# Performance work log

Hardware: AMD Instinct MI355X
Metric: run time of the kernel (lower is better)

The kernel has to match this reference:

```python
import jax, jax.numpy as jnp
import numpy as np
from jax import lax

B, C, H, W = 2, 64, 48, 64
RU, RV = 3, 3
U, V = 2 * RU + 1, 2 * RV + 1
D = U * V  # 49 displacements


def setup_inputs() -> dict:
    key = jax.random.key(0)
    ks = jax.random.split(key, 12)
    p = lambda k, shape, s: jax.random.normal(k, shape, jnp.float32) * s
    feat1 = p(ks[0], (B, C, H, W), 1.0)
    feat2 = p(ks[1], (B, C, H, W), 1.0)
    gy, gx = jnp.meshgrid(jnp.arange(H, dtype=jnp.float32), jnp.arange(W, dtype=jnp.float32), indexing='ij')
    base = jnp.broadcast_to(jnp.stack([gx, gy])[None], (B, 2, H, W))  # channel0=x, channel1=y
    coords = base + p(ks[2], (B, 2, H, W), 1.5)
    return {
        'feat1': feat1, 'feat2': feat2, 'coords': coords,
        # MatchingNet (ConvBlock = conv+ReLU, BN folded into conv)
        'w0': p(ks[3], (96, 2 * C, 3, 3), 0.06), 'b0': jnp.zeros((96,), jnp.float32),
        'w1': p(ks[4], (128, 96, 3, 3), 0.05), 'b1': jnp.zeros((128,), jnp.float32),
        'w2': p(ks[5], (128, 128, 3, 3), 0.04), 'b2': jnp.zeros((128,), jnp.float32),
        'w3': p(ks[6], (64, 128, 3, 3), 0.04), 'b3': jnp.zeros((64,), jnp.float32),
        'wd': p(ks[7], (32, 64, 4, 4), 0.05), 'bd': jnp.zeros((32,), jnp.float32),  # deconv k4 s2 p1
        'w5': p(ks[8], (1, 32, 3, 3), 0.1), 'b5': jnp.zeros((1,), jnp.float32),
        # Displacement-aware projection: 1x1 conv over the 49 displacement channels
        'wdap': p(ks[9], (D, D), 0.15),
    }


def _conv(x, w, b, stride=1, pad=1):
    y = lax.conv_general_dilated(x, w, (stride, stride), ((pad, pad), (pad, pad)),
                                 dimension_numbers=('NCHW', 'OIHW', 'NCHW'))
    return y + b[None, :, None, None]


def _warp_with_context(feat2, coords):
    # grid_sample(bilinear, zeros padding, align_corners=True) at coords + every displacement
    b, c, h, w = feat2.shape
    du = jnp.arange(-RU, RU + 1, dtype=feat2.dtype)
    dv = jnp.arange(-RV, RV + 1, dtype=feat2.dtype)
    x = coords[:, 0][:, None, None, :, :] + du[None, None, :, None, None]  # (b,V,U,h,w) via broadcast
    y = coords[:, 1][:, None, None, :, :] + dv[None, :, None, None, None]
    x0 = jnp.floor(x); y0 = jnp.floor(y)
    wx = (x - x0)[:, None]; wy = (y - y0)[:, None]  # (b,1,V,U,h,w)
    x0i = x0.astype(jnp.int32); y0i = y0.astype(jnp.int32)
    feat_flat = feat2.reshape(b, c, h * w)

    def gather(xi, yi):
        valid = (xi >= 0) & (xi < w) & (yi >= 0) & (yi < h)
        idx = jnp.clip(yi, 0, h - 1) * w + jnp.clip(xi, 0, w - 1)
        v = jax.vmap(lambda f, i: f[:, i])(feat_flat, idx.reshape(b, -1))  # (b,c,P)
        v = v.reshape(b, c, V, U, h, w)
        return v * valid[:, None].astype(feat2.dtype)

    v00 = gather(x0i, y0i)
    v01 = gather(x0i + 1, y0i)
    v10 = gather(x0i, y0i + 1)
    v11 = gather(x0i + 1, y0i + 1)
    out = v00 * (1 - wx) * (1 - wy) + v01 * wx * (1 - wy) + v10 * (1 - wx) * wy + v11 * wx * wy
    return out.transpose(0, 2, 3, 1, 4, 5)  # (b, V, U, c, h, w)


def reference(feat1, feat2, coords, w0, b0, w1, b1, w2, b2, w3, b3, wd, bd, w5, b5, wdap):
    b, c, h, w = feat1.shape
    f2 = _warp_with_context(feat2, coords)
    f1 = jnp.broadcast_to(feat1[:, None, None], (b, V, U, c, h, w))
    feat = jnp.concatenate([f1, f2], axis=3).reshape(b * V * U, 2 * c, h, w)
    # MatchingNet
    x = jnp.maximum(_conv(feat, w0, b0), 0)
    x = jnp.maximum(_conv(x, w1, b1, stride=2), 0)
    x = jnp.maximum(_conv(x, w2, b2), 0)
    x = jnp.maximum(_conv(x, w3, b3), 0)
    x = lax.conv_general_dilated(x, wd, (1, 1), ((2, 2), (2, 2)), lhs_dilation=(2, 2),
                                 dimension_numbers=('NCHW', 'OIHW', 'NCHW')) + bd[None, :, None, None]
    x = jnp.maximum(x, 0)
    cost = _conv(x, w5, b5).reshape(b, V, U, h, w)
    # DAP: 1x1 conv across the D displacement channels, no bias
    cost = jnp.einsum('ed,bdhw->behw', wdap, cost.reshape(b, D, h, w)).reshape(b, V, U, h, w)
    prob = jax.nn.softmax(cost.reshape(b, D, h, w), axis=1).reshape(b, V, U, h, w)
    du = jnp.arange(-RU, RU + 1, dtype=feat1.dtype)
    dv = jnp.arange(-RV, RV + 1, dtype=feat1.dtype)
    dx = jnp.sum(prob * du[None, None, :, None, None], axis=(1, 2))
    dy = jnp.sum(prob * dv[None, :, None, None, None], axis=(1, 2))
    return coords + jnp.stack([dx, dy], axis=1)
```

## Files before the change

kernel.cpp:

```cpp
#include <hip/hip_runtime.h>
#include <hip/hip_bf16.h>

using bf16 = __hip_bfloat16;
typedef __attribute__((ext_vector_type(8))) __bf16 bf16x8;
typedef __attribute__((ext_vector_type(4))) float f32x4;

static __device__ __forceinline__ bf16 f2b(float v) { return __float2bfloat16(v); }
static __device__ __forceinline__ float us2f(unsigned short u) {
    return __uint_as_float(((unsigned)u) << 16);
}


__global__ void sentinel_k(float* __restrict__ out, int nel, float val) {
    int i = blockIdx.x * 256 + threadIdx.x;
    if (i < nel) out[i] = val;
}

__global__ void pack_all(const float* __restrict__ w0, const float* __restrict__ w1,
                         const float* __restrict__ w2, const float* __restrict__ w3,
                         const float* __restrict__ wd, bf16* __restrict__ wsw0,
                         bf16* __restrict__ wsw0a, bf16* __restrict__ wsw1,
                         bf16* __restrict__ wsw2, bf16* __restrict__ wsw3,
                         bf16* __restrict__ wswd) {
    int i = blockIdx.x * 256 + threadIdx.x;
    if (i < 110592) {
        int icbase = (i < 55296) ? 64 : 0;
        bf16* dst = (i < 55296) ? wsw0 : wsw0a;
        int o = (i < 55296) ? i : i - 55296;
        int j = o & 7, lane = (o >> 3) & 63;
        int m = lane & 15, q = lane >> 4;
        int cc = (o >> 9) & 1;
        int fragid = o >> 10;
        int t = fragid / 6, ocf = fragid % 6;
        int oc = ocf * 16 + m, ic = cc * 32 + q * 8 + j;
        dst[o] = f2b(w0[((size_t)oc * 128 + icbase + ic) * 9 + t]);
    } else if (i < 307200) {
        int o = i - 110592;
        int j = o & 7, lane = (o >> 3) & 63;
        int m = lane & 15, q = lane >> 4;
        int cc = (o >> 9) % 12;
        int fragid = (o >> 9) / 12;
        int t2 = fragid / 8, ocf = fragid % 8;
        int oc = ocf * 16 + m;
        int pc = cc * 32 + q * 8 + j;
        int dy = (t2 < 2) ? -1 : 0;
        int dx = (t2 & 1) ? 0 : -1;
        int p = pc / 96, ic = pc % 96;
        int py = p >> 1, px = p & 1;
        int ky = (dy == -1) ? (py == 1 ? 0 : -1) : (py == 0 ? 1 : 2);
        int kx = (dx == -1) ? (px == 1 ? 0 : -1) : (px == 0 ? 1 : 2);
        float v = (ky >= 0 && kx >= 0) ? w1[((size_t)oc * 96 + ic) * 9 + ky * 3 + kx] : 0.f;
        wsw1[o] = f2b(v);
    } else if (i < 454656) {
        int o = i - 307200;
        int j = o & 7, lane = (o >> 3) & 63;
        int m = lane & 15, q = lane >> 4;
        int cc = (o >> 9) % 4;
        int fragid = (o >> 9) / 4;
        int t = fragid / 8, ocf = fragid % 8;
        int oc = ocf * 16 + m, ic = cc * 32 + q * 8 + j;
        wsw2[o] = f2b(w2[((size_t)oc * 128 + ic) * 9 + t]);
    } else if (i < 528384) {
        int o = i - 454656;
        int j = o & 7, lane = (o >> 3) & 63;
        int m = lane & 15, q = lane >> 4;
        int cc = (o >> 9) % 4;
        int fragid = (o >> 9) / 4;
        int t = fragid / 4, ocf = fragid % 4;
        int oc = ocf * 16 + m, ic = cc * 32 + q * 8 + j;
        wsw3[o] = f2b(w3[((size_t)oc * 128 + ic) * 9 + t]);
    } else if (i < 561152) {
        int o = i - 528384;
        int j = o & 7, lane = (o >> 3) & 63;
        int m = lane & 15, q = lane >> 4;
        int cc = (o >> 9) & 1;
        int ocf = (o >> 10) & 1;
        int t2 = (o >> 11) & 3;
        int c = o >> 13;
        int oc = ocf * 16 + m, ic = cc * 32 + q * 8 + j;
        int qy = c >> 1, qx = c & 1;
        int dy = qy - 1 + (t2 >> 1), dx = qx - 1 + (t2 & 1);
        int ky = (qy == 0) ? (dy == -1 ? 0 : 2) : (dy == 0 ? 1 : 3);
        int kx = (qx == 0) ? (dx == -1 ? 0 : 2) : (dx == 0 ? 1 : 3);
        wswd[o] = f2b(wd[((size_t)oc * 64 + ic) * 16 + ky * 4 + kx]);
    }
}

__global__ void to_nhwc2(const float* __restrict__ feat1, const float* __restrict__ feat2,
                         bf16* __restrict__ f1n, bf16* __restrict__ f2n) {
    int i = blockIdx.x * 256 + threadIdx.x;
    const float* src = (i < 393216) ? feat1 : feat2;
    bf16* dst = (i < 393216) ? f1n : f2n;
    int o = (i < 393216) ? i : i - 393216;
    if (o >= 393216) return;
    int c = o & 63;
    int p = (o >> 6) % 3072;
    int b = o / (3072 * 64);
    dst[o] = f2b(src[((size_t)b * 64 + c) * 3072 + p]);
}

__global__ __launch_bounds__(256) void warp_kernel(const bf16* __restrict__ f2n,
                                                   const float* __restrict__ coords,
                                                   bf16* __restrict__ f2w, int bd0, int cnt) {
    int idx = blockIdx.x * 256 + threadIdx.x;
    if (idx >= cnt * 3072 * 8) return;
    int g = idx & 7;
    int pix = idx >> 3;
    int p = pix % 3072;
    int z = pix / 3072;
    int bd = bd0 + z;
    int b = bd / 49, d = bd % 49;
    float du = (float)(d % 7 - 3), dv = (float)(d / 7 - 3);
    float cx = coords[(size_t)(b * 2 + 0) * 3072 + p] + du;
    float cy = coords[(size_t)(b * 2 + 1) * 3072 + p] + dv;
    float x0f = floorf(cx), y0f = floorf(cy);
    float wx = cx - x0f, wy = cy - y0f;
    int x0 = (int)x0f, y0 = (int)y0f;
    int x1 = x0 + 1, y1 = y0 + 1;
    bool vx0 = (x0 >= 0) && (x0 < 64), vx1 = (x1 >= 0) && (x1 < 64);
    bool vy0 = (y0 >= 0) && (y0 < 48), vy1 = (y1 >= 0) && (y1 < 48);
    int xc0 = min(max(x0, 0), 63), xc1 = min(max(x1, 0), 63);
    int yc0 = min(max(y0, 0), 47), yc1 = min(max(y1, 0), 47);
    float w00 = (vx0 && vy0) ? (1.f - wx) * (1.f - wy) : 0.f;
    float w01 = (vx1 && vy0) ? wx * (1.f - wy) : 0.f;
    float w10 = (vx0 && vy1) ? (1.f - wx) * wy : 0.f;
    float w11 = (vx1 && vy1) ? wx * wy : 0.f;
    const unsigned short* f2 = (const unsigned short*)f2n + (size_t)b * 3072 * 64 + g * 8;
    ushort4 a0 = *(const ushort4*)(f2 + (size_t)(yc0 * 64 + xc0) * 64);
    ushort4 a1 = *(const ushort4*)(f2 + (size_t)(yc0 * 64 + xc0) * 64 + 4);
    ushort4 b0v = *(const ushort4*)(f2 + (size_t)(yc0 * 64 + xc1) * 64);
    ushort4 b1v = *(const ushort4*)(f2 + (size_t)(yc0 * 64 + xc1) * 64 + 4);
    ushort4 c0 = *(const ushort4*)(f2 + (size_t)(yc1 * 64 + xc0) * 64);
    ushort4 c1 = *(const ushort4*)(f2 + (size_t)(yc1 * 64 + xc0) * 64 + 4);
    ushort4 d0 = *(const ushort4*)(f2 + (size_t)(yc1 * 64 + xc1) * 64);
    ushort4 d1 = *(const ushort4*)(f2 + (size_t)(yc1 * 64 + xc1) * 64 + 4);
    unsigned short ua[8] = {a0.x, a0.y, a0.z, a0.w, a1.x, a1.y, a1.z, a1.w};
    unsigned short ub[8] = {b0v.x, b0v.y, b0v.z, b0v.w, b1v.x, b1v.y, b1v.z, b1v.w};
    unsigned short uc[8] = {c0.x, c0.y, c0.z, c0.w, c1.x, c1.y, c1.z, c1.w};
    unsigned short ud[8] = {d0.x, d0.y, d0.z, d0.w, d1.x, d1.y, d1.z, d1.w};
    unsigned short ro[8];
#pragma unroll
    for (int e = 0; e < 8; ++e) {
        float v = w00 * us2f(ua[e]) + w01 * us2f(ub[e]) + w10 * us2f(uc[e]) + w11 * us2f(ud[e]);
        bf16 r = f2b(v);
        ro[e] = *(unsigned short*)&r;
    }
    unsigned short* outp = (unsigned short*)f2w + ((size_t)z * 3072 + p) * 64 + g * 8;
    *(ushort4*)outp = (ushort4){ro[0], ro[1], ro[2], ro[3]};
    *(ushort4*)(outp + 4) = (ushort4){ro[4], ro[5], ro[6], ro[7]};
}

template <int IC, int OCTOT, int OC_BLK, int H, int W, int MROWS, int NTAPS, int DXW,
          int DYLO, int DXLO, int BMODE, int OMODE>
__global__ __launch_bounds__(256, 4) void conv_px4(const bf16* __restrict__ in_,
                                                   const bf16* __restrict__ wsw_,
                                                   const float* __restrict__ bias,
                                                   const bf16* __restrict__ base_,
                                                   bf16* __restrict__ out, int bd0) {
    constexpr int NCH = IC / 32;
    constexpr int NfT = OC_BLK / 16;
    constexpr int TPXQ = MROWS * W / 4;
    constexpr int MF = TPXQ / 16;
    constexpr int NDY = NTAPS / DXW;
    constexpr int ROWS_IN = MROWS + NDY - 1;
    constexpr int COLS_IN = W + DXW - 1;
    constexpr int NOCF = OCTOT / 16;
    constexpr int PITCH = 40;
    constexpr int SZA = ROWS_IN * COLS_IN * PITCH;
    constexpr int OUTSH = MROWS * W * OC_BLK;
    constexpr int SMEM = (SZA > OUTSH) ? SZA : OUTSH;
    __shared__ __align__(16) unsigned short s_mem[SMEM];

    const unsigned short* in = (const unsigned short*)in_;
    const unsigned short* wsw = (const unsigned short*)wsw_;
    const unsigned short* baseh = (const unsigned short*)base_;
    const int tid = threadIdx.x;
    const int wp = tid >> 6, lane = tid & 63;
    const int m = lane & 15, q = lane >> 4;
    const int bx = blockIdx.x, by = blockIdx.y, z = blockIdx.z;
    const int foff = m * PITCH + q * 8;
    const int ocbase = by * OC_BLK;

    f32x4 acc[MF][NfT];
#pragma unroll
    for (int a = 0; a < MF; ++a)
#pragma unroll
        for (int nf = 0; nf < NfT; ++nf) acc[a][nf] = (f32x4){0.f, 0.f, 0.f, 0.f};

    for (int cc = 0; cc < NCH; ++cc) {
        constexpr int SZE = ROWS_IN * COLS_IN * 4;
        for (int i = tid; i < SZE; i += 256) {
            int e = i & 3;
            int pix = i >> 2;
            int cI = pix % COLS_IN;
            int rr = pix / COLS_IN;
            int gy = bx * MROWS + rr + DYLO;
            int gx = cI + DXLO;
            uint4 v = {0u, 0u, 0u, 0u};
            if (gy >= 0 && gy < H && gx >= 0 && gx < W)
                v = *(const uint4*)(in + ((size_t)(z * H + gy) * W + gx) * IC + cc * 32 + e * 8);
            *(uint4*)(&s_mem[pix * PITCH + e * 8]) = v;
        }
        __syncthreads();
        {
            bf16x8 bcur[NfT], bnxt[NfT];
#pragma unroll
            for (int nf = 0; nf < NfT; ++nf) {
                const int fragoc = (ocbase >> 4) + nf;
                bcur[nf] = *(const bf16x8*)(wsw + (((size_t)0 * NOCF + fragoc) * NCH + cc) * 512 +
                                            lane * 8);
            }
#pragma unroll
            for (int t = 0; t < NTAPS; ++t) {
                if (t + 1 < NTAPS) {
#pragma unroll
                    for (int nf = 0; nf < NfT; ++nf) {
                        const int fragoc = (ocbase >> 4) + nf;
                        bnxt[nf] = *(const bf16x8*)(wsw +
                                                    (((size_t)(t + 1) * NOCF + fragoc) * NCH + cc) *
                                                        512 +
                                                    lane * 8);
                    }
                }
                bf16x8 af[MF];
#pragma unroll
                for (int mf = 0; mf < MF; ++mf) {
                    const int pxb = wp * TPXQ + mf * 16;
                    const int yl = pxb / W, xb = pxb % W;
                    const unsigned short* pa =
                        &s_mem[((yl + t / DXW) * COLS_IN + xb + t % DXW) * PITCH] + foff;
                    af[mf] = *(const bf16x8*)pa;
                }
#pragma unroll
                for (int mf = 0; mf < MF; ++mf)
#pragma unroll
                    for (int nf = 0; nf < NfT; ++nf)
                        acc[mf][nf] = __builtin_amdgcn_mfma_f32_16x16x32_bf16(af[mf], bcur[nf],
                                                                              acc[mf][nf], 0, 0, 0);
                if (t + 1 < NTAPS) {
#pragma unroll
                    for (int nf = 0; nf < NfT; ++nf) bcur[nf] = bnxt[nf];
                }
            }
        }
        __syncthreads();
    }

    const int bimg = (bd0 + z) / 49;
    float bb[NfT];
    if constexpr (BMODE == 0) {
#pragma unroll
        for (int nf = 0; nf < NfT; ++nf) bb[nf] = bias[ocbase + nf * 16 + m];
    }
#pragma unroll
    for (int mf = 0; mf < MF; ++mf) {
        const int pxb = wp * TPXQ + mf * 16;
#pragma unroll
        for (int r = 0; r < 4; ++r) {
            const int px = pxb + q * 4 + r;
            const int yl = px / W, xl = px % W;
            const int gy = bx * MROWS + yl;
#pragma unroll
            for (int nf = 0; nf < NfT; ++nf) {
                const int oc = nf * 16 + m;
                float v = acc[mf][nf][r];
                if constexpr (BMODE == 1)
                    v += us2f(baseh[(((size_t)bimg * 48 + gy) * 64 + xl) * 96 + ocbase + oc]);
                else
                    v += bb[nf];
                if constexpr (OMODE != 4) v = fmaxf(v, 0.f);
                bf16 bv = f2b(v);
                s_mem[px * OC_BLK + oc] = *(unsigned short*)&bv;
            }
        }
    }
    __syncthreads();
    constexpr int TOT16 = MROWS * W * OC_BLK / 8;
    for (int g = tid; g < TOT16; g += 256) {
        const int o = g * 8;
        if constexpr (OMODE == 1) {
            const int xx = o / 384;
            const int rr = o % 384;
            const int pp = rr / 96;
            const int oco = rr % 96;
            const int px = (pp >> 1) * 64 + 2 * xx + (pp & 1);
            uint4 vv = *(const uint4*)&s_mem[px * 96 + oco];
            *(uint4*)((unsigned short*)out + (((size_t)z * 24 + bx) * 32 + xx) * 384 + rr) = vv;
        } else {
            uint4 vv = *(const uint4*)&s_mem[o];
            const int px = o / OC_BLK;
            const int oco = o % OC_BLK;
            const int gy = bx * MROWS + px / W;
            const int xl = px % W;
            *(uint4*)((unsigned short*)out + (((size_t)z * H + gy) * W + xl) * OCTOT + ocbase +
                      oco) = vv;
        }
    }
}

__global__ __launch_bounds__(256, 4) void deconv_c4(const bf16* __restrict__ in_,
                                                    const bf16* __restrict__ wswd_,
                                                    const float* __restrict__ bias,
                                                    bf16* __restrict__ out) {
    constexpr int PITCH = 40;
    __shared__ __align__(16) unsigned short s_mem[16384];

    const unsigned short* in = (const unsigned short*)in_;
    const unsigned short* wsw = (const unsigned short*)wswd_;
    const int tid = threadIdx.x;
    const int cls = tid >> 6, lane = tid & 63;
    const int m = lane & 15, q = lane >> 4;
    const int qy = cls >> 1, qx = cls & 1;
    const int bx = blockIdx.x;
    const int z = blockIdx.y;
    const int foff = m * PITCH + q * 8;

    f32x4 acc[8][2];
#pragma unroll
    for (int a = 0; a < 8; ++a) {
        acc[a][0] = (f32x4){0.f, 0.f, 0.f, 0.f};
        acc[a][1] = (f32x4){0.f, 0.f, 0.f, 0.f};
    }

    for (int cc = 0; cc < 2; ++cc) {
        constexpr int SZE = 6 * 34 * 4;
        for (int i = tid; i < SZE; i += 256) {
            int e = i & 3;
            int pix = i >> 2;
            int cI = pix % 34;
            int rr = pix / 34;
            int gy = bx * 4 + rr - 1;
            int gx = cI - 1;
            uint4 v = {0u, 0u, 0u, 0u};
            if (gy >= 0 && gy < 24 && gx >= 0 && gx < 32)
                v = *(const uint4*)(in + ((size_t)(z * 24 + gy) * 32 + gx) * 64 + cc * 32 + e * 8);
            *(uint4*)(&s_mem[pix * PITCH + e * 8]) = v;
        }
        __syncthreads();
        {
            bf16x8 bcur[2], bnxt[2];
#pragma unroll
            for (int nf = 0; nf < 2; ++nf)
                bcur[nf] = *(const bf16x8*)(wsw + cls * 8192 + nf * 1024 + cc * 512 + lane * 8);
#pragma unroll
            for (int t = 0; t < 4; ++t) {
                if (t + 1 < 4) {
#pragma unroll
                    for (int nf = 0; nf < 2; ++nf)
                        bnxt[nf] = *(const bf16x8*)(wsw + cls * 8192 + (t + 1) * 2048 + nf * 1024 +
                                                    cc * 512 + lane * 8);
                }
                const int dy = qy - 1 + (t >> 1);
                const int dx = qx - 1 + (t & 1);
                bf16x8 af[8];
#pragma unroll
                for (int mf = 0; mf < 8; ++mf) {
                    const int yl = mf >> 1, xb = (mf & 1) * 16;
                    const unsigned short* pa =
                        &s_mem[((yl + dy + 1) * 34 + xb + dx + 1) * PITCH] + foff;
                    af[mf] = *(const bf16x8*)pa;
                }
#pragma unroll
                for (int mf = 0; mf < 8; ++mf)
#pragma unroll
                    for (int nf = 0; nf < 2; ++nf)
                        acc[mf][nf] = __builtin_amdgcn_mfma_f32_16x16x32_bf16(af[mf], bcur[nf],
                                                                              acc[mf][nf], 0, 0, 0);
                if (t + 1 < 4) {
                    bcur[0] = bnxt[0];
                    bcur[1] = bnxt[1];
                }
            }
        }
        __syncthreads();
    }

    const float bb0 = bias[m], bb1 = bias[16 + m];
#pragma unroll
    for (int mf = 0; mf < 8; ++mf) {
#pragma unroll
        for (int r = 0; r < 4; ++r) {
            const int px = mf * 16 + q * 4 + r;
            const int yl = px >> 5, xl = px & 31;
            const int opx = (2 * yl + qy) * 64 + 2 * xl + qx;
            float v0 = fmaxf(acc[mf][0][r] + bb0, 0.f);
            float v1 = fmaxf(acc[mf][1][r] + bb1, 0.f);
            bf16 b0 = f2b(v0), b1 = f2b(v1);
            s_mem[opx * 32 + m] = *(unsigned short*)&b0;
            s_mem[opx * 32 + 16 + m] = *(unsigned short*)&b1;
        }
    }
    __syncthreads();
    for (int g = tid; g < 2048; g += 256) {
        const int o = g * 8;
        *(uint4*)((unsigned short*)out + ((size_t)z * 3072 + bx * 512) * 32 + o) =
            *(const uint4*)&s_mem[o];
    }
}

__global__ __launch_bounds__(256) void conv5_k(const bf16* __restrict__ in_,
                                               const float* __restrict__ w5,
                                               const float* __restrict__ b5,
                                               float* __restrict__ cost, int bd0, int cnt) {
    __shared__ float s_w5[9][32];
    const int tid = threadIdx.x;
    for (int i = tid; i < 288; i += 256) {
        int ic = i % 32, t = i / 32;
        s_w5[t][ic] = w5[ic * 9 + t];
    }
    __syncthreads();
    int idx = blockIdx.x * 256 + tid;
    if (idx >= cnt * 3072) return;
    int p = idx % 3072, z = idx / 3072;
    int y = p >> 6, x = p & 63;
    const unsigned short* in = (const unsigned short*)in_;
    float acc = b5[0];
#pragma unroll
    for (int ky = 0; ky < 3; ++ky) {
        int gy = y + ky - 1;
        if (gy < 0 || gy >= 48) continue;
#pragma unroll
        for (int kx = 0; kx < 3; ++kx) {
            int gx = x + kx - 1;
            if (gx < 0 || gx >= 64) continue;
            const ushort4* src = (const ushort4*)(in + ((size_t)(z * 48 + gy) * 64 + gx) * 32);
            const float* wr = s_w5[ky * 3 + kx];
#pragma unroll
            for (int e = 0; e < 8; ++e) {
                ushort4 u = src[e];
                acc = fmaf(us2f(u.x), wr[e * 4 + 0], acc);
                acc = fmaf(us2f(u.y), wr[e * 4 + 1], acc);
                acc = fmaf(us2f(u.z), wr[e * 4 + 2], acc);
                acc = fmaf(us2f(u.w), wr[e * 4 + 3], acc);
            }
        }
    }
    cost[(size_t)(bd0 + z) * 3072 + p] = acc;
}

__global__ __launch_bounds__(256) void dap_flow(const float* __restrict__ cost,
                                                const float* __restrict__ wdap,
                                                const float* __restrict__ coords,
                                                float* __restrict__ outp) {
    __shared__ float s_w[49 * 49];
    int tid = threadIdx.x;
    for (int i = tid; i < 2401; i += 256) s_w[i] = wdap[i];
    __syncthreads();
    int idx = blockIdx.x * 256 + tid;
    if (idx >= 2 * 3072) return;
    int p = idx % 3072, b = idx / 3072;
    float c[49];
#pragma unroll
    for (int d = 0; d < 49; ++d) c[d] = cost[((size_t)(b * 49 + d)) * 3072 + p];
    float mx = -1e30f;
    for (int e = 0; e < 49; ++e) {
        float s = 0.f;
#pragma unroll
        for (int d = 0; d < 49; ++d) s = fmaf(s_w[e * 49 + d], c[d], s);
        mx = fmaxf(mx, s);
    }
    float sum = 0.f, sx = 0.f, sy = 0.f;
    for (int e = 0; e < 49; ++e) {
        float s = 0.f;
#pragma unroll
        for (int d = 0; d < 49; ++d) s = fmaf(s_w[e * 49 + d], c[d], s);
        float pr = __expf(s - mx);
        sum += pr;
        sx += pr * (float)(e % 7 - 3);
        sy += pr * (float)(e / 7 - 3);
    }
    float inv = 1.f / sum;
    outp[(size_t)(b * 2 + 0) * 3072 + p] = coords[(size_t)(b * 2 + 0) * 3072 + p] + sx * inv;
    outp[(size_t)(b * 2 + 1) * 3072 + p] = coords[(size_t)(b * 2 + 1) * 3072 + p] + sy * inv;
}

extern "C" void kernel_launch(void* const* d_in, const int* in_sizes, int n_in,
                              void* d_out, int out_size, void* d_ws, size_t ws_size,
                              hipStream_t stream) {
    (void)in_sizes; (void)n_in;
    const float* feat1 = (const float*)d_in[0];
    const float* feat2 = (const float*)d_in[1];
    const float* coords = (const float*)d_in[2];
    const float* w0 = (const float*)d_in[3];
    const float* b0 = (const float*)d_in[4];
    const float* w1 = (const float*)d_in[5];
    const float* b1 = (const float*)d_in[6];
    const float* w2 = (const float*)d_in[7];
    const float* b2 = (const float*)d_in[8];
    const float* w3 = (const float*)d_in[9];
    const float* b3 = (const float*)d_in[10];
    const float* wd = (const float*)d_in[11];
    const float* bdc = (const float*)d_in[12];
    const float* w5 = (const float*)d_in[13];
    const float* b5 = (const float*)d_in[14];
    const float* wdap = (const float*)d_in[15];
    float* outp = (float*)d_out;

    char* ws = (char*)d_ws;
    bf16* wsw0 = (bf16*)(ws + 0);
    bf16* wsw0a = (bf16*)(ws + 110592);
    bf16* wsw1 = (bf16*)(ws + 221184);
    bf16* wsw2 = (bf16*)(ws + 614400);
    bf16* wsw3 = (bf16*)(ws + 909312);
    bf16* wswd = (bf16*)(ws + 1056768);
    bf16* f1n = (bf16*)(ws + 1122304);
    bf16* part0 = (bf16*)(ws + 1908736);
    float* cost = (float*)(ws + 3088384);
    bf16* f2n = (bf16*)(ws + 4292608);
    const size_t fixed_end = 5079040;

    const int cand[7] = {98, 49, 25, 14, 7, 2, 1};
    int nb = 0;
    for (int i = 0; i < 7; ++i) {
        if (fixed_end + (size_t)983040 * cand[i] <= ws_size) { nb = cand[i]; break; }
    }
    if (nb == 0) {
        float val = 10000.f + (float)(ws_size >> 20);
        sentinel_k<<<dim3((out_size + 255) / 256), 256, 0, stream>>>(outp, out_size, val);
        return;
    }
    char* regA = ws + fixed_end;
    char* regB = regA + (size_t)393216 * nb;
    bf16* f2w = (bf16*)regA;
    bf16* x1 = (bf16*)regA;
    bf16* x3 = (bf16*)regA;
    bf16* x0p = (bf16*)regB;
    bf16* x2 = (bf16*)regB;
    bf16* xd = (bf16*)regB;

    pack_all<<<dim3(2192), 256, 0, stream>>>(w0, w1, w2, w3, wd, wsw0, wsw0a, wsw1, wsw2, wsw3,
                                             wswd);
    to_nhwc2<<<dim3(3072), 256, 0, stream>>>(feat1, feat2, f1n, f2n);
    conv_px4<64, 96, 96, 48, 64, 2, 9, 3, -1, -1, 0, 4>
        <<<dim3(24, 1, 2), 256, 0, stream>>>(f1n, wsw0a, b0, nullptr, part0, 0);

    for (int s = 0; s < 98; s += nb) {
        int cnt = (98 - s < nb) ? (98 - s) : nb;
        warp_kernel<<<dim3(cnt * 96), 256, 0, stream>>>(f2n, coords, f2w, s, cnt);
        conv_px4<64, 96, 96, 48, 64, 2, 9, 3, -1, -1, 1, 1>
            <<<dim3(24, 1, cnt), 256, 0, stream>>>(f2w, wsw0, nullptr, part0, x0p, s);
        conv_px4<384, 128, 64, 24, 32, 4, 4, 2, -1, -1, 0, 0>
            <<<dim3(6, 2, cnt), 256, 0, stream>>>(x0p, wsw1, b1, nullptr, x1, s);
        conv_px4<128, 128, 64, 24, 32, 4, 9, 3, -1, -1, 0, 0>
            <<<dim3(6, 2, cnt), 256, 0, stream>>>(x1, wsw2, b2, nullptr, x2, s);
        conv_px4<128, 64, 64, 24, 32, 4, 9, 3, -1, -1, 0, 0>
            <<<dim3(6, 1, cnt), 256, 0, stream>>>(x2, wsw3, b3, nullptr, x3, s);
        deconv_c4<<<dim3(6, cnt), 256, 0, stream>>>(x3, wswd, bdc, xd);
        conv5_k<<<dim3(cnt * 12), 256, 0, stream>>>(xd, w5, b5, cost, s, cnt);
    }

    dap_flow<<<dim3(24), 256, 0, stream>>>(cost, wdap, coords, outp);
}
```

Baseline: 369.7 us.

## Fuse bilinear warp into first conv and stage wider channel slabs per sync

The separate warp kernel is removed. The first MatchingNet conv now computes the bilinear samples of feat2 directly while filling its shared-memory tile, so the warped tensor is never written to or read back from global memory. The conv kernels stage 64 or 96 input channels per shared-memory fill instead of 32, which cuts the number of barrier-separated load phases and lets weight prefetch run across the whole K loop. The packing and NHWC-conversion kernels are merged into one prologue launch. In exchange the halo pixels of each tile are warped redundantly, shared-memory use per block grows, and occupancy may drop.

```diff
diff --git a/kernel.cpp b/kernel.cpp
--- a/kernel.cpp
+++ b/kernel.cpp
@@ -16,12 +16,14 @@
     if (i < nel) out[i] = val;
 }
 
-__global__ void pack_all(const float* __restrict__ w0, const float* __restrict__ w1,
-                         const float* __restrict__ w2, const float* __restrict__ w3,
-                         const float* __restrict__ wd, bf16* __restrict__ wsw0,
-                         bf16* __restrict__ wsw0a, bf16* __restrict__ wsw1,
-                         bf16* __restrict__ wsw2, bf16* __restrict__ wsw3,
-                         bf16* __restrict__ wswd) {
+__global__ void prologue_k(const float* __restrict__ w0, const float* __restrict__ w1,
+                           const float* __restrict__ w2, const float* __restrict__ w3,
+                           const float* __restrict__ wd, const float* __restrict__ feat1,
+                           const float* __restrict__ feat2, bf16* __restrict__ wsw0,
+                           bf16* __restrict__ wsw0a, bf16* __restrict__ wsw1,
+                           bf16* __restrict__ wsw2, bf16* __restrict__ wsw3,
+                           bf16* __restrict__ wswd, bf16* __restrict__ f1n,
+                           bf16* __restrict__ f2n) {
     int i = blockIdx.x * 256 + threadIdx.x;
     if (i < 110592) {
         int icbase = (i < 55296) ? 64 : 0;
@@ -83,81 +85,31 @@
         int ky = (qy == 0) ? (dy == -1 ? 0 : 2) : (dy == 0 ? 1 : 3);
         int kx = (qx == 0) ? (dx == -1 ? 0 : 2) : (dx == 0 ? 1 : 3);
         wswd[o] = f2b(wd[((size_t)oc * 64 + ic) * 16 + ky * 4 + kx]);
-    }
-}
-
-__global__ void to_nhwc2(const float* __restrict__ feat1, const float* __restrict__ feat2,
-                         bf16* __restrict__ f1n, bf16* __restrict__ f2n) {
-    int i = blockIdx.x * 256 + threadIdx.x;
-    const float* src = (i < 393216) ? feat1 : feat2;
-    bf16* dst = (i < 393216) ? f1n : f2n;
-    int o = (i < 393216) ? i : i - 393216;
-    if (o >= 393216) return;
-    int c = o & 63;
-    int p = (o >> 6) % 3072;
-    int b = o / (3072 * 64);
-    dst[o] = f2b(src[((size_t)b * 64 + c) * 3072 + p]);
-}
-
-__global__ __launch_bounds__(256) void warp_kernel(const bf16* __restrict__ f2n,
-                                                   const float* __restrict__ coords,
-                                                   bf16* __restrict__ f2w, int bd0, int cnt) {
-    int idx = blockIdx.x * 256 + threadIdx.x;
-    if (idx >= cnt * 3072 * 8) return;
-    int g = idx & 7;
-    int pix = idx >> 3;
-    int p = pix % 3072;
-    int z = pix / 3072;
-    int bd = bd0 + z;
-    int b = bd / 49, d = bd % 49;
-    float du = (float)(d % 7 - 3), dv = (float)(d / 7 - 3);
-    float cx = coords[(size_t)(b * 2 + 0) * 3072 + p] + du;
-    float cy = coords[(size_t)(b * 2 + 1) * 3072 + p] + dv;
-    float x0f = floorf(cx), y0f = floorf(cy);
-    float wx = cx - x0f, wy = cy - y0f;
-    int x0 = (int)x0f, y0 = (int)y0f;
-    int x1 = x0 + 1, y1 = y0 + 1;
-    bool vx0 = (x0 >= 0) && (x0 < 64), vx1 = (x1 >= 0) && (x1 < 64);
-    bool vy0 = (y0 >= 0) && (y0 < 48), vy1 = (y1 >= 0) && (y1 < 48);
-    int xc0 = min(max(x0, 0), 63), xc1 = min(max(x1, 0), 63);
-    int yc0 = min(max(y0, 0), 47), yc1 = min(max(y1, 0), 47);
-    float w00 = (vx0 && vy0) ? (1.f - wx) * (1.f - wy) : 0.f;
-    float w01 = (vx1 && vy0) ? wx * (1.f - wy) : 0.f;
-    float w10 = (vx0 && vy1) ? (1.f - wx) * wy : 0.f;
-    float w11 = (vx1 && vy1) ? wx * wy : 0.f;
-    const unsigned short* f2 = (const unsigned short*)f2n + (size_t)b * 3072 * 64 + g * 8;
-    ushort4 a0 = *(const ushort4*)(f2 + (size_t)(yc0 * 64 + xc0) * 64);
-    ushort4 a1 = *(const ushort4*)(f2 + (size_t)(yc0 * 64 + xc0) * 64 + 4);
-    ushort4 b0v = *(const ushort4*)(f2 + (size_t)(yc0 * 64 + xc1) * 64);
-    ushort4 b1v = *(const ushort4*)(f2 + (size_t)(yc0 * 64 + xc1) * 64 + 4);
-    ushort4 c0 = *(const ushort4*)(f2 + (size_t)(yc1 * 64 + xc0) * 64);
-    ushort4 c1 = *(const ushort4*)(f2 + (size_t)(yc1 * 64 + xc0) * 64 + 4);
-    ushort4 d0 = *(const ushort4*)(f2 + (size_t)(yc1 * 64 + xc1) * 64);
-    ushort4 d1 = *(const ushort4*)(f2 + (size_t)(yc1 * 64 + xc1) * 64 + 4);
-    unsigned short ua[8] = {a0.x, a0.y, a0.z, a0.w, a1.x, a1.y, a1.z, a1.w};
-    unsigned short ub[8] = {b0v.x, b0v.y, b0v.z, b0v.w, b1v.x, b1v.y, b1v.z, b1v.w};
-    unsigned short uc[8] = {c0.x, c0.y, c0.z, c0.w, c1.x, c1.y, c1.z, c1.w};
-    unsigned short ud[8] = {d0.x, d0.y, d0.z, d0.w, d1.x, d1.y, d1.z, d1.w};
-    unsigned short ro[8];
-#pragma unroll
-    for (int e = 0; e < 8; ++e) {
-        float v = w00 * us2f(ua[e]) + w01 * us2f(ub[e]) + w10 * us2f(uc[e]) + w11 * us2f(ud[e]);
-        bf16 r = f2b(v);
-        ro[e] = *(unsigned short*)&r;
-    }
-    unsigned short* outp = (unsigned short*)f2w + ((size_t)z * 3072 + p) * 64 + g * 8;
-    *(ushort4*)outp = (ushort4){ro[0], ro[1], ro[2], ro[3]};
-    *(ushort4*)(outp + 4) = (ushort4){ro[4], ro[5], ro[6], ro[7]};
-}
-
-template <int IC, int OCTOT, int OC_BLK, int H, int W, int MROWS, int NTAPS, int DXW,
-          int DYLO, int DXLO, int BMODE, int OMODE>
-__global__ __launch_bounds__(256, 4) void conv_px4(const bf16* __restrict__ in_,
-                                                   const bf16* __restrict__ wsw_,
-                                                   const float* __restrict__ bias,
-                                                   const bf16* __restrict__ base_,
-                                                   bf16* __restrict__ out, int bd0) {
-    constexpr int NCH = IC / 32;
+    } else if (i < 561152 + 786432) {
+        int o2 = i - 561152;
+        const float* src = (o2 < 393216) ? feat1 : feat2;
+        bf16* dst = (o2 < 393216) ? f1n : f2n;
+        int o = (o2 < 393216) ? o2 : o2 - 393216;
+        int c = o & 63;
+        int p = (o >> 6) % 3072;
+        int b = o / (3072 * 64);
+        dst[o] = f2b(src[((size_t)b * 64 + c) * 3072 + p]);
+    }
+}
+
+template <int IC, int ICS, int OCTOT, int OC_BLK, int H, int W, int MROWS, int NTAPS,
+          int DXW, int DYLO, int DXLO, int BMODE, int OMODE, int WARPIN>
+__global__ __launch_bounds__(256, 4) void conv_fz(const bf16* __restrict__ in_,
+                                                  const bf16* __restrict__ wsw_,
+                                                  const float* __restrict__ bias,
+                                                  const bf16* __restrict__ base_,
+                                                  bf16* __restrict__ out, int bd0,
+                                                  const float* __restrict__ coords) {
+    constexpr int NST = IC / ICS;
+    constexpr int ICSC = ICS / 32;
+    constexpr int KSTEPS = NTAPS * ICSC;
+    constexpr int TOTS = NST * KSTEPS;
+    constexpr int ICS8 = ICS / 8;
     constexpr int NfT = OC_BLK / 16;
     constexpr int TPXQ = MROWS * W / 4;
     constexpr int MF = TPXQ / 16;
@@ -165,8 +117,9 @@
     constexpr int ROWS_IN = MROWS + NDY - 1;
     constexpr int COLS_IN = W + DXW - 1;
     constexpr int NOCF = OCTOT / 16;
-    constexpr int PITCH = 40;
-    constexpr int SZA = ROWS_IN * COLS_IN * PITCH;
+    constexpr int NCH = IC / 32;
+    constexpr int PITCHC = ICS + 8;
+    constexpr int SZA = ROWS_IN * COLS_IN * PITCHC;
     constexpr int OUTSH = MROWS * W * OC_BLK;
     constexpr int SMEM = (SZA > OUTSH) ? SZA : OUTSH;
     __shared__ __align__(16) unsigned short s_mem[SMEM];
@@ -178,75 +131,128 @@
     const int wp = tid >> 6, lane = tid & 63;
     const int m = lane & 15, q = lane >> 4;
     const int bx = blockIdx.x, by = blockIdx.y, z = blockIdx.z;
-    const int foff = m * PITCH + q * 8;
+    const int foff = m * PITCHC + q * 8;
     const int ocbase = by * OC_BLK;
 
+    const int bd = bd0 + z;
+    const int bimg = bd / 49;
+    const int disp = bd % 49;
+    const float du = (float)(disp % 7 - 3), dv = (float)(disp / 7 - 3);
+
     f32x4 acc[MF][NfT];
 #pragma unroll
     for (int a = 0; a < MF; ++a)
 #pragma unroll
         for (int nf = 0; nf < NfT; ++nf) acc[a][nf] = (f32x4){0.f, 0.f, 0.f, 0.f};
 
-    for (int cc = 0; cc < NCH; ++cc) {
-        constexpr int SZE = ROWS_IN * COLS_IN * 4;
+    bf16x8 bcur[NfT], bnxt[NfT];
+#pragma unroll
+    for (int nf = 0; nf < NfT; ++nf) {
+        const int fragoc = (ocbase >> 4) + nf;
+        bcur[nf] = *(const bf16x8*)(wsw + ((size_t)fragoc * NCH) * 512 + lane * 8);
+    }
+
+#pragma unroll
+    for (int ss = 0; ss < NST; ++ss) {
+        constexpr int SZE = ROWS_IN * COLS_IN * ICS8;
         for (int i = tid; i < SZE; i += 256) {
-            int e = i & 3;
-            int pix = i >> 2;
-            int cI = pix % COLS_IN;
-            int rr = pix / COLS_IN;
-            int gy = bx * MROWS + rr + DYLO;
-            int gx = cI + DXLO;
-            uint4 v = {0u, 0u, 0u, 0u};
-            if (gy >= 0 && gy < H && gx >= 0 && gx < W)
-                v = *(const uint4*)(in + ((size_t)(z * H + gy) * W + gx) * IC + cc * 32 + e * 8);
-            *(uint4*)(&s_mem[pix * PITCH + e * 8]) = v;
-        }
-        __syncthreads();
-        {
-            bf16x8 bcur[NfT], bnxt[NfT];
-#pragma unroll
-            for (int nf = 0; nf < NfT; ++nf) {
-                const int fragoc = (ocbase >> 4) + nf;
-                bcur[nf] = *(const bf16x8*)(wsw + (((size_t)0 * NOCF + fragoc) * NCH + cc) * 512 +
-                                            lane * 8);
-            }
-#pragma unroll
-            for (int t = 0; t < NTAPS; ++t) {
-                if (t + 1 < NTAPS) {
-#pragma unroll
-                    for (int nf = 0; nf < NfT; ++nf) {
-                        const int fragoc = (ocbase >> 4) + nf;
-                        bnxt[nf] = *(const bf16x8*)(wsw +
-                                                    (((size_t)(t + 1) * NOCF + fragoc) * NCH + cc) *
-                                                        512 +
-                                                    lane * 8);
+            int e, pix;
+            if constexpr ((ICS8 & (ICS8 - 1)) == 0) {
+                e = i & (ICS8 - 1);
+                pix = i / ICS8;
+            } else {
+                e = i % ICS8;
+                pix = i / ICS8;
+            }
+            const int cI = pix % COLS_IN;
+            const int rr = pix / COLS_IN;
+            const int gy = bx * MROWS + rr + DYLO;
+            const int gx = cI + DXLO;
+            if constexpr (WARPIN) {
+                unsigned short ro[8] = {0, 0, 0, 0, 0, 0, 0, 0};
+                if (gy >= 0 && gy < H && gx >= 0 && gx < W) {
+                    const int p = gy * 64 + gx;
+                    float cx = coords[(size_t)(bimg * 2 + 0) * 3072 + p] + du;
+                    float cy = coords[(size_t)(bimg * 2 + 1) * 3072 + p] + dv;
+                    float x0f = floorf(cx), y0f = floorf(cy);
+                    float wx = cx - x0f, wy = cy - y0f;
+                    int x0 = (int)x0f, y0 = (int)y0f;
+                    int x1 = x0 + 1, y1 = y0 + 1;
+                    bool vx0 = (x0 >= 0) && (x0 < 64), vx1 = (x1 >= 0) && (x1 < 64);
+                    bool vy0 = (y0 >= 0) && (y0 < 48), vy1 = (y1 >= 0) && (y1 < 48);
+                    int xc0 = min(max(x0, 0), 63), xc1 = min(max(x1, 0), 63);
+                    int yc0 = min(max(y0, 0), 47), yc1 = min(max(y1, 0), 47);
+                    float w00 = (vx0 && vy0) ? (1.f - wx) * (1.f - wy) : 0.f;
+                    float w01 = (vx1 && vy0) ? wx * (1.f - wy) : 0.f;
+                    float w10 = (vx0 && vy1) ? (1.f - wx) * wy : 0.f;
+                    float w11 = (vx1 && vy1) ? wx * wy : 0.f;
+                    const unsigned short* f2 = in + (size_t)bimg * 196608 + e * 8;
+                    const uint4 ua = *(const uint4*)(f2 + (size_t)(yc0 * 64 + xc0) * 64);
+                    const uint4 ub = *(const uint4*)(f2 + (size_t)(yc0 * 64 + xc1) * 64);
+                    const uint4 uc = *(const uint4*)(f2 + (size_t)(yc1 * 64 + xc0) * 64);
+                    const uint4 ud = *(const uint4*)(f2 + (size_t)(yc1 * 64 + xc1) * 64);
+                    const unsigned short* pa = (const unsigned short*)&ua;
+                    const unsigned short* pb = (const unsigned short*)&ub;
+                    const unsigned short* pc = (const unsigned short*)&uc;
+                    const unsigned short* pd = (const unsigned short*)&ud;
+#pragma unroll
+                    for (int ee = 0; ee < 8; ++ee) {
+                        float v = w00 * us2f(pa[ee]) + w01 * us2f(pb[ee]) +
+                                  w10 * us2f(pc[ee]) + w11 * us2f(pd[ee]);
+                        bf16 r = f2b(v);
+                        ro[ee] = *(unsigned short*)&r;
                     }
                 }
-                bf16x8 af[MF];
-#pragma unroll
-                for (int mf = 0; mf < MF; ++mf) {
-                    const int pxb = wp * TPXQ + mf * 16;
-                    const int yl = pxb / W, xb = pxb % W;
-                    const unsigned short* pa =
-                        &s_mem[((yl + t / DXW) * COLS_IN + xb + t % DXW) * PITCH] + foff;
-                    af[mf] = *(const bf16x8*)pa;
+                *(uint4*)(&s_mem[pix * PITCHC + e * 8]) = *(const uint4*)ro;
+            } else {
+                uint4 v = {0u, 0u, 0u, 0u};
+                if (gy >= 0 && gy < H && gx >= 0 && gx < W)
+                    v = *(const uint4*)(in + ((size_t)(z * H + gy) * W + gx) * IC + ss * ICS +
+                                        e * 8);
+                *(uint4*)(&s_mem[pix * PITCHC + e * 8]) = v;
+            }
+        }
+        __syncthreads();
+#pragma unroll
+        for (int k = 0; k < KSTEPS; ++k) {
+            const int s = ss * KSTEPS + k;
+            if (s + 1 < TOTS) {
+                const int sn = s + 1;
+                const int ssn = sn / KSTEPS, kn = sn % KSTEPS;
+                const int tn = kn / ICSC, c32n = kn % ICSC;
+                const int ccgn = ssn * ICSC + c32n;
+#pragma unroll
+                for (int nf = 0; nf < NfT; ++nf) {
+                    const int fragoc = (ocbase >> 4) + nf;
+                    bnxt[nf] = *(const bf16x8*)(wsw +
+                                                (((size_t)tn * NOCF + fragoc) * NCH + ccgn) * 512 +
+                                                lane * 8);
                 }
-#pragma unroll
-                for (int mf = 0; mf < MF; ++mf)
-#pragma unroll
-                    for (int nf = 0; nf < NfT; ++nf)
-                        acc[mf][nf] = __builtin_amdgcn_mfma_f32_16x16x32_bf16(af[mf], bcur[nf],
-                                                                              acc[mf][nf], 0, 0, 0);
-                if (t + 1 < NTAPS) {
-#pragma unroll
-                    for (int nf = 0; nf < NfT; ++nf) bcur[nf] = bnxt[nf];
-                }
+            }
+            const int t = k / ICSC, c32 = k % ICSC;
+            bf16x8 af[MF];
+#pragma unroll
+            for (int mf = 0; mf < MF; ++mf) {
+                const int pxb = wp * TPXQ + mf * 16;
+                const int yl = pxb / W, xb = pxb % W;
+                const unsigned short* pa =
+                    &s_mem[((yl + t / DXW) * COLS_IN + xb + t % DXW) * PITCHC + c32 * 32] + foff;
+                af[mf] = *(const bf16x8*)pa;
+            }
+#pragma unroll
+            for (int mf = 0; mf < MF; ++mf)
+#pragma unroll
+                for (int nf = 0; nf < NfT; ++nf)
+                    acc[mf][nf] =
+                        __builtin_amdgcn_mfma_f32_16x16x32_bf16(af[mf], bcur[nf], acc[mf][nf], 0, 0, 0);
+            if (s + 1 < TOTS) {
+#pragma unroll
+                for (int nf = 0; nf < NfT; ++nf) bcur[nf] = bnxt[nf];
             }
         }
         __syncthreads();
     }
 
-    const int bimg = (bd0 + z) / 49;
     float bb[NfT];
     if constexpr (BMODE == 0) {
 #pragma unroll
@@ -302,7 +308,8 @@
                                                     const bf16* __restrict__ wswd_,
                                                     const float* __restrict__ bias,
                                                     bf16* __restrict__ out) {
-    constexpr int PITCH = 40;
+    constexpr int PITCHC = 72;
+    constexpr int SZA = 6 * 34 * PITCHC;
     __shared__ __align__(16) unsigned short s_mem[16384];
 
     const unsigned short* in = (const unsigned short*)in_;
@@ -313,7 +320,7 @@
     const int qy = cls >> 1, qx = cls & 1;
     const int bx = blockIdx.x;
     const int z = blockIdx.y;
-    const int foff = m * PITCH + q * 8;
+    const int foff = m * PITCHC + q * 8;
 
     f32x4 acc[8][2];
 #pragma unroll
@@ -322,58 +329,58 @@
         acc[a][1] = (f32x4){0.f, 0.f, 0.f, 0.f};
     }
 
-    for (int cc = 0; cc < 2; ++cc) {
-        constexpr int SZE = 6 * 34 * 4;
-        for (int i = tid; i < SZE; i += 256) {
-            int e = i & 3;
-            int pix = i >> 2;
-            int cI = pix % 34;
-            int rr = pix / 34;
-            int gy = bx * 4 + rr - 1;
-            int gx = cI - 1;
-            uint4 v = {0u, 0u, 0u, 0u};
-            if (gy >= 0 && gy < 24 && gx >= 0 && gx < 32)
-                v = *(const uint4*)(in + ((size_t)(z * 24 + gy) * 32 + gx) * 64 + cc * 32 + e * 8);
-            *(uint4*)(&s_mem[pix * PITCH + e * 8]) = v;
-        }
-        __syncthreads();
-        {
-            bf16x8 bcur[2], bnxt[2];
-#pragma unroll
-            for (int nf = 0; nf < 2; ++nf)
-                bcur[nf] = *(const bf16x8*)(wsw + cls * 8192 + nf * 1024 + cc * 512 + lane * 8);
-#pragma unroll
-            for (int t = 0; t < 4; ++t) {
-                if (t + 1 < 4) {
-#pragma unroll
-                    for (int nf = 0; nf < 2; ++nf)
-                        bnxt[nf] = *(const bf16x8*)(wsw + cls * 8192 + (t + 1) * 2048 + nf * 1024 +
-                                                    cc * 512 + lane * 8);
-                }
-                const int dy = qy - 1 + (t >> 1);
-                const int dx = qx - 1 + (t & 1);
-                bf16x8 af[8];
-#pragma unroll
-                for (int mf = 0; mf < 8; ++mf) {
-                    const int yl = mf >> 1, xb = (mf & 1) * 16;
-                    const unsigned short* pa =
-                        &s_mem[((yl + dy + 1) * 34 + xb + dx + 1) * PITCH] + foff;
-                    af[mf] = *(const bf16x8*)pa;
-                }
-#pragma unroll
-                for (int mf = 0; mf < 8; ++mf)
-#pragma unroll
-                    for (int nf = 0; nf < 2; ++nf)
-                        acc[mf][nf] = __builtin_amdgcn_mfma_f32_16x16x32_bf16(af[mf], bcur[nf],
-                                                                              acc[mf][nf], 0, 0, 0);
-                if (t + 1 < 4) {
-                    bcur[0] = bnxt[0];
-                    bcur[1] = bnxt[1];
-                }
-            }
-        }
-        __syncthreads();
-    }
+    constexpr int SZE = 6 * 34 * 8;
+    for (int i = tid; i < SZE; i += 256) {
+        int e = i & 7;
+        int pix = i >> 3;
+        int cI = pix % 34;
+        int rr = pix / 34;
+        int gy = bx * 4 + rr - 1;
+        int gx = cI - 1;
+        uint4 v = {0u, 0u, 0u, 0u};
+        if (gy >= 0 && gy < 24 && gx >= 0 && gx < 32)
+            v = *(const uint4*)(in + ((size_t)(z * 24 + gy) * 32 + gx) * 64 + e * 8);
+        *(uint4*)(&s_mem[pix * PITCHC + e * 8]) = v;
+    }
+    __syncthreads();
+    {
+        bf16x8 bcur[2], bnxt[2];
+#pragma unroll
+        for (int nf = 0; nf < 2; ++nf)
+            bcur[nf] = *(const bf16x8*)(wsw + cls * 8192 + nf * 1024 + lane * 8);
+#pragma unroll
+        for (int s = 0; s < 8; ++s) {
+            if (s + 1 < 8) {
+                const int tn = (s + 1) >> 1, ccn = (s + 1) & 1;
+#pragma unroll
+                for (int nf = 0; nf < 2; ++nf)
+                    bnxt[nf] = *(const bf16x8*)(wsw + cls * 8192 + tn * 2048 + nf * 1024 +
+                                                ccn * 512 + lane * 8);
+            }
+            const int t = s >> 1, cc = s & 1;
+            const int dy = qy - 1 + (t >> 1);
+            const int dx = qx - 1 + (t & 1);
+            bf16x8 af[8];
+#pragma unroll
+            for (int mf = 0; mf < 8; ++mf) {
+                const int yl = mf >> 1, xb = (mf & 1) * 16;
+                const unsigned short* pa =
+                    &s_mem[((yl + dy + 1) * 34 + xb + dx + 1) * PITCHC + cc * 32] + foff;
+                af[mf] = *(const bf16x8*)pa;
+            }
+#pragma unroll
+            for (int mf = 0; mf < 8; ++mf)
+#pragma unroll
+                for (int nf = 0; nf < 2; ++nf)
+                    acc[mf][nf] =
+                        __builtin_amdgcn_mfma_f32_16x16x32_bf16(af[mf], bcur[nf], acc[mf][nf], 0, 0, 0);
+            if (s + 1 < 8) {
+                bcur[0] = bnxt[0];
+                bcur[1] = bnxt[1];
+            }
+        }
+    }
+    __syncthreads();
 
     const float bb0 = bias[m], bb1 = bias[16 + m];
 #pragma unroll
@@ -521,30 +528,27 @@
     }
     char* regA = ws + fixed_end;
     char* regB = regA + (size_t)393216 * nb;
-    bf16* f2w = (bf16*)regA;
     bf16* x1 = (bf16*)regA;
     bf16* x3 = (bf16*)regA;
     bf16* x0p = (bf16*)regB;
     bf16* x2 = (bf16*)regB;
     bf16* xd = (bf16*)regB;
 
-    pack_all<<<dim3(2192), 256, 0, stream>>>(w0, w1, w2, w3, wd, wsw0, wsw0a, wsw1, wsw2, wsw3,
-                                             wswd);
-    to_nhwc2<<<dim3(3072), 256, 0, stream>>>(feat1, feat2, f1n, f2n);
-    conv_px4<64, 96, 96, 48, 64, 2, 9, 3, -1, -1, 0, 4>
-        <<<dim3(24, 1, 2), 256, 0, stream>>>(f1n, wsw0a, b0, nullptr, part0, 0);
+    prologue_k<<<dim3(5265), 256, 0, stream>>>(w0, w1, w2, w3, wd, feat1, feat2, wsw0, wsw0a,
+                                               wsw1, wsw2, wsw3, wswd, f1n, f2n);
+    conv_fz<64, 64, 96, 96, 48, 64, 2, 9, 3, -1, -1, 0, 4, 0>
+        <<<dim3(24, 1, 2), 256, 0, stream>>>(f1n, wsw0a, b0, nullptr, part0, 0, nullptr);
 
     for (int s = 0; s < 98; s += nb) {
         int cnt = (98 - s < nb) ? (98 - s) : nb;
-        warp_kernel<<<dim3(cnt * 96), 256, 0, stream>>>(f2n, coords, f2w, s, cnt);
-        conv_px4<64, 96, 96, 48, 64, 2, 9, 3, -1, -1, 1, 1>
-            <<<dim3(24, 1, cnt), 256, 0, stream>>>(f2w, wsw0, nullptr, part0, x0p, s);
-        conv_px4<384, 128, 64, 24, 32, 4, 4, 2, -1, -1, 0, 0>
-            <<<dim3(6, 2, cnt), 256, 0, stream>>>(x0p, wsw1, b1, nullptr, x1, s);
-        conv_px4<128, 128, 64, 24, 32, 4, 9, 3, -1, -1, 0, 0>
-            <<<dim3(6, 2, cnt), 256, 0, stream>>>(x1, wsw2, b2, nullptr, x2, s);
-        conv_px4<128, 64, 64, 24, 32, 4, 9, 3, -1, -1, 0, 0>
-            <<<dim3(6, 1, cnt), 256, 0, stream>>>(x2, wsw3, b3, nullptr, x3, s);
+        conv_fz<64, 64, 96, 96, 48, 64, 2, 9, 3, -1, -1, 1, 1, 1>
+            <<<dim3(24, 1, cnt), 256, 0, stream>>>(f2n, wsw0, nullptr, part0, x0p, s, coords);
+        conv_fz<384, 96, 128, 64, 24, 32, 4, 4, 2, -1, -1, 0, 0, 0>
+            <<<dim3(6, 2, cnt), 256, 0, stream>>>(x0p, wsw1, b1, nullptr, x1, s, nullptr);
+        conv_fz<128, 64, 128, 64, 24, 32, 4, 9, 3, -1, -1, 0, 0, 0>
+            <<<dim3(6, 2, cnt), 256, 0, stream>>>(x1, wsw2, b2, nullptr, x2, s, nullptr);
+        conv_fz<128, 64, 64, 64, 24, 32, 4, 9, 3, -1, -1, 0, 0, 0>
+            <<<dim3(6, 1, cnt), 256, 0, stream>>>(x2, wsw3, b3, nullptr, x3, s, nullptr);
         deconv_c4<<<dim3(6, cnt), 256, 0, stream>>>(x3, wswd, bdc, xd);
         conv5_k<<<dim3(cnt * 12), 256, 0, stream>>>(xd, w5, b5, cost, s, cnt);
     }
```

Result: slower. 419.8 us (+13.5%).

## Parallelize DAP softmax across wavefront lanes and fuse prologue kernels

Applied to the files above, without the earlier changes.

The final DAP+softmax-expectation kernel now assigns one wavefront per pixel, with each lane computing one projected displacement and shuffle reductions for the max and sums, instead of one thread per pixel doing all 2×49×49 FMAs. This replaces a 24-block launch with 1536 blocks to raise parallelism on that tail stage. The weight packing and NHWC conversion kernels are merged into one launch to save launch overhead. Each block reloads the 49×49 weight matrix into shared memory, which adds redundant global traffic.

```diff
diff --git a/kernel.cpp b/kernel.cpp
--- a/kernel.cpp
+++ b/kernel.cpp
@@ -16,12 +16,14 @@
     if (i < nel) out[i] = val;
 }
 
-__global__ void pack_all(const float* __restrict__ w0, const float* __restrict__ w1,
-                         const float* __restrict__ w2, const float* __restrict__ w3,
-                         const float* __restrict__ wd, bf16* __restrict__ wsw0,
-                         bf16* __restrict__ wsw0a, bf16* __restrict__ wsw1,
-                         bf16* __restrict__ wsw2, bf16* __restrict__ wsw3,
-                         bf16* __restrict__ wswd) {
+__global__ void prologue_k(const float* __restrict__ w0, const float* __restrict__ w1,
+                           const float* __restrict__ w2, const float* __restrict__ w3,
+                           const float* __restrict__ wd, const float* __restrict__ feat1,
+                           const float* __restrict__ feat2, bf16* __restrict__ wsw0,
+                           bf16* __restrict__ wsw0a, bf16* __restrict__ wsw1,
+                           bf16* __restrict__ wsw2, bf16* __restrict__ wsw3,
+                           bf16* __restrict__ wswd, bf16* __restrict__ f1n,
+                           bf16* __restrict__ f2n) {
     int i = blockIdx.x * 256 + threadIdx.x;
     if (i < 110592) {
         int icbase = (i < 55296) ? 64 : 0;
@@ -83,20 +85,16 @@
         int ky = (qy == 0) ? (dy == -1 ? 0 : 2) : (dy == 0 ? 1 : 3);
         int kx = (qx == 0) ? (dx == -1 ? 0 : 2) : (dx == 0 ? 1 : 3);
         wswd[o] = f2b(wd[((size_t)oc * 64 + ic) * 16 + ky * 4 + kx]);
-    }
-}
-
-__global__ void to_nhwc2(const float* __restrict__ feat1, const float* __restrict__ feat2,
-                         bf16* __restrict__ f1n, bf16* __restrict__ f2n) {
-    int i = blockIdx.x * 256 + threadIdx.x;
-    const float* src = (i < 393216) ? feat1 : feat2;
-    bf16* dst = (i < 393216) ? f1n : f2n;
-    int o = (i < 393216) ? i : i - 393216;
-    if (o >= 393216) return;
-    int c = o & 63;
-    int p = (o >> 6) % 3072;
-    int b = o / (3072 * 64);
-    dst[o] = f2b(src[((size_t)b * 64 + c) * 3072 + p]);
+    } else if (i < 561152 + 786432) {
+        int o2 = i - 561152;
+        const float* src = (o2 < 393216) ? feat1 : feat2;
+        bf16* dst = (o2 < 393216) ? f1n : f2n;
+        int o = (o2 < 393216) ? o2 : o2 - 393216;
+        int c = o & 63;
+        int p = (o >> 6) % 3072;
+        int b = o / (3072 * 64);
+        dst[o] = f2b(src[((size_t)b * 64 + c) * 3072 + p]);
+    }
 }
 
 __global__ __launch_bounds__(256) void warp_kernel(const bf16* __restrict__ f2n,
@@ -438,40 +436,45 @@
     cost[(size_t)(bd0 + z) * 3072 + p] = acc;
 }
 
-__global__ __launch_bounds__(256) void dap_flow(const float* __restrict__ cost,
-                                                const float* __restrict__ wdap,
-                                                const float* __restrict__ coords,
-                                                float* __restrict__ outp) {
-    __shared__ float s_w[49 * 49];
-    int tid = threadIdx.x;
+__global__ __launch_bounds__(256) void dap_flow_w(const float* __restrict__ cost,
+                                                  const float* __restrict__ wdap,
+                                                  const float* __restrict__ coords,
+                                                  float* __restrict__ outp) {
+    __shared__ float s_w[2401];
+    __shared__ float s_c[4][52];
+    const int tid = threadIdx.x;
+    const int w = tid >> 6, lane = tid & 63;
+    const int idx = blockIdx.x * 4 + w;
+    const int p = idx % 3072, b = idx / 3072;
     for (int i = tid; i < 2401; i += 256) s_w[i] = wdap[i];
+    if (lane < 49) s_c[w][lane] = cost[((size_t)(b * 49 + lane)) * 3072 + p];
     __syncthreads();
-    int idx = blockIdx.x * 256 + tid;
-    if (idx >= 2 * 3072) return;
-    int p = idx % 3072, b = idx / 3072;
-    float c[49];
-#pragma unroll
-    for (int d = 0; d < 49; ++d) c[d] = cost[((size_t)(b * 49 + d)) * 3072 + p];
-    float mx = -1e30f;
-    for (int e = 0; e < 49; ++e) {
-        float s = 0.f;
-#pragma unroll
-        for (int d = 0; d < 49; ++d) s = fmaf(s_w[e * 49 + d], c[d], s);
-        mx = fmaxf(mx, s);
-    }
-    float sum = 0.f, sx = 0.f, sy = 0.f;
-    for (int e = 0; e < 49; ++e) {
-        float s = 0.f;
-#pragma unroll
-        for (int d = 0; d < 49; ++d) s = fmaf(s_w[e * 49 + d], c[d], s);
-        float pr = __expf(s - mx);
-        sum += pr;
-        sx += pr * (float)(e % 7 - 3);
-        sy += pr * (float)(e / 7 - 3);
-    }
-    float inv = 1.f / sum;
-    outp[(size_t)(b * 2 + 0) * 3072 + p] = coords[(size_t)(b * 2 + 0) * 3072 + p] + sx * inv;
-    outp[(size_t)(b * 2 + 1) * 3072 + p] = coords[(size_t)(b * 2 + 1) * 3072 + p] + sy * inv;
+    float s = -1e30f;
+    if (lane < 49) {
+        s = 0.f;
+        const float* wr = &s_w[lane * 49];
+        const float* cr = s_c[w];
+#pragma unroll
+        for (int d = 0; d < 49; ++d) s = fmaf(wr[d], cr[d], s);
+    }
+    float mx = s;
+#pragma unroll
+    for (int off = 32; off; off >>= 1) mx = fmaxf(mx, __shfl_xor(mx, off));
+    float pr = (lane < 49) ? __expf(s - mx) : 0.f;
+    float sum = pr;
+    float sx = pr * (float)(lane % 7 - 3);
+    float sy = pr * (float)(lane / 7 - 3);
+#pragma unroll
+    for (int off = 32; off; off >>= 1) {
+        sum += __shfl_xor(sum, off);
+        sx += __shfl_xor(sx, off);
+        sy += __shfl_xor(sy, off);
+    }
+    if (lane == 0) {
+        float inv = 1.f / sum;
+        outp[(size_t)(b * 2 + 0) * 3072 + p] = coords[(size_t)(b * 2 + 0) * 3072 + p] + sx * inv;
+        outp[(size_t)(b * 2 + 1) * 3072 + p] = coords[(size_t)(b * 2 + 1) * 3072 + p] + sy * inv;
+    }
 }
 
 extern "C" void kernel_launch(void* const* d_in, const int* in_sizes, int n_in,
@@ -528,9 +531,8 @@
     bf16* x2 = (bf16*)regB;
     bf16* xd = (bf16*)regB;
 
-    pack_all<<<dim3(2192), 256, 0, stream>>>(w0, w1, w2, w3, wd, wsw0, wsw0a, wsw1, wsw2, wsw3,
-                                             wswd);
-    to_nhwc2<<<dim3(3072), 256, 0, stream>>>(feat1, feat2, f1n, f2n);
+    prologue_k<<<dim3(5265), 256, 0, stream>>>(w0, w1, w2, w3, wd, feat1, feat2, wsw0, wsw0a,
+                                               wsw1, wsw2, wsw3, wswd, f1n, f2n);
     conv_px4<64, 96, 96, 48, 64, 2, 9, 3, -1, -1, 0, 4>
         <<<dim3(24, 1, 2), 256, 0, stream>>>(f1n, wsw0a, b0, nullptr, part0, 0);
 
@@ -549,5 +551,5 @@
         conv5_k<<<dim3(cnt * 12), 256, 0, stream>>>(xd, w5, b5, cost, s, cnt);
     }
 
-    dap_flow<<<dim3(24), 256, 0, stream>>>(cost, wdap, coords, outp);
-}
+    dap_flow_w<<<dim3(1536), 256, 0, stream>>>(cost, wdap, coords, outp);
+}
```

Measured after the change: 332.1 us (median of 2 runs). 10.2% less time.
